# Kernel tuning notes

Measured on AMD Instinct MI355X. Metric: run time of the kernel, lower is better.

Reference implementation:

```python
import jax, jax.numpy as jnp
import numpy as np

THRESH = 1.0
TAU_M = 20.0
TAU_S = 5.0
NUM_STEPS = 300
CFG = (34 * 34 * 2, 800, 10)
BATCH = 32
SPIKE_PROB = 0.02


def _dtdu(um, us, spike):
    # dt/du = 1 / (du/dt) at spike time; du/dt = -um/tau_m + us/tau_s,
    # magnitude clamped away from zero for numerical safety.
    dudt = -um / TAU_M + us / TAU_S
    dudt = jnp.where(dudt >= 0, jnp.maximum(dudt, 1e-2), jnp.minimum(dudt, -1e-2))
    return spike / dudt


def _forward(input, W1, W2, batch_size):
    dm = jnp.exp(jnp.float32(-1.0 / TAU_M))
    ds = jnp.exp(jnp.float32(-1.0 / TAU_S))
    Din, H, O = CFG
    # (B,2,34,34,T) -> (T,B,Din)
    x = jnp.moveaxis(input.reshape(batch_size, Din, NUM_STEPS), -1, 0)
    z = lambda d: jnp.zeros((batch_size, d), jnp.float32)
    carry = (
        jnp.ones((batch_size, H), jnp.float32), z(Din), z(Din),   # sav1, vm1, vs1
        jnp.ones((batch_size, O), jnp.float32), z(H), z(H),       # sav2, vm2, vs2
        jnp.full((batch_size, O), float(NUM_STEPS), jnp.float32), # out_t
        z(O),                                                     # out_u
        jnp.zeros((3,), jnp.float32),                             # sum_sp
        jnp.zeros((batch_size, H, Din), jnp.float32),             # h1_v
        jnp.zeros((batch_size, O, H), jnp.float32),               # h2_v
        jnp.zeros((batch_size, H, Din), jnp.float32),             # h1_dvdt
        jnp.zeros((batch_size, O, H), jnp.float32),               # h2_dvdt
        z(H), z(O),                                               # h1_dtdu, h2_dtdu
    )

    def step(c, xs):
        (sav1, vm1, vs1, sav2, vm2, vs2, out_t, out_u, sum_sp,
         h1_v, h2_v, h1_dvdt, h2_dvdt, h1_dtdu, h2_dtdu) = c
        in_spike, t = xs
        # layer 1 NOSO neuron (dual-exponential kernel, single spike via sav gate)
        vm1 = vm1 * dm + in_spike
        vs1 = vs1 * ds + in_spike
        um1 = vm1 @ W1.T
        us1 = vs1 @ W1.T
        u1 = sav1 * (um1 - us1)
        spk1 = (u1 >= THRESH).astype(jnp.float32)
        sav1 = sav1 * (1.0 - spk1)
        # layer 2 (output neuron)
        vm2 = vm2 * dm + spk1
        vs2 = vs2 * ds + spk1
        um2 = vm2 @ W2.T
        us2 = vs2 @ W2.T
        u2 = sav2 * (um2 - us2)
        spk2 = (u2 >= THRESH).astype(jnp.float32)
        sav2 = sav2 * (1.0 - spk2)
        # spike-time / potential readout
        out_t = out_t + spk2 * (t.astype(jnp.float32) - NUM_STEPS)
        out_u = out_u + spk2 * u2
        sum_sp = sum_sp + jnp.stack([in_spike.sum(), spk1.sum(), spk2.sum()])
        # outer-product stat accumulation (B,out,in)
        h1_v = h1_v + spk1[:, :, None] * (vm1 - vs1)[:, None, :]
        h2_v = h2_v + spk2[:, :, None] * (vm2 - vs2)[:, None, :]
        h1_dvdt = h1_dvdt + spk1[:, :, None] * (vm1 / TAU_M - vs1 / TAU_S)[:, None, :]
        h2_dvdt = h2_dvdt + spk2[:, :, None] * (vm2 / TAU_M - vs2 / TAU_S)[:, None, :]
        h1_dtdu = h1_dtdu + _dtdu(um1, us1, spk1)
        h2_dtdu = h2_dtdu + _dtdu(um2, us2, spk2)
        return (sav1, vm1, vs1, sav2, vm2, vs2, out_t, out_u, sum_sp,
                h1_v, h2_v, h1_dvdt, h2_dvdt, h1_dtdu, h2_dtdu), None

    c, _ = jax.lax.scan(step, carry, (x, jnp.arange(NUM_STEPS)))
    out_t, out_u, sum_sp = c[6], c[7], c[8]
    h1_v, h2_v, h1_dvdt, h2_dvdt, h1_dtdu, h2_dtdu = c[9], c[10], c[11], c[12], c[13], c[14]
    return out_t, out_u, sum_sp, h1_v, h2_v, h1_dvdt, h2_dvdt, h1_dtdu, h2_dtdu


def setup_inputs() -> dict:
    key = jax.random.key(0)
    k1, k2, k3 = jax.random.split(key, 3)
    inp = (jax.random.uniform(k1, (BATCH, 2, 34, 34, NUM_STEPS)) < SPIKE_PROB).astype(jnp.float32)
    W1 = jax.random.normal(k2, (CFG[1], CFG[0]), jnp.float32) * float(np.sqrt(2.0 / CFG[0]))
    W2 = jax.random.normal(k3, (CFG[2], CFG[1]), jnp.float32) * float(np.sqrt(2.0 / CFG[1]))
    return {"input": inp, "W1": W1, "W2": W2, "batch_size": BATCH}


def reference(input, W1, W2, batch_size):
    return _forward(input, W1, W2, batch_size)
```

## Files before the change

kernel.cpp:

```cpp
#include <hip/hip_runtime.h>
#include <cstdint>
#include <cstddef>

#define BB 32
#define TT 300
#define DD 2312
#define HH 800
#define OO 10
#define CAP1 128
#define KMAX 32

typedef float f32x4 __attribute__((ext_vector_type(4)));

#define DM_F 0.95122942450071400909f
#define DS_F 0.81873075307798185867f

#define OUT_T_OFF 0
#define OUT_U_OFF 320
#define SUM_OFF   640
#define H1V_OFF   643ull
#define H2V_OFF   59187843ull
#define H1DV_OFF  59443843ull
#define H2DV_OFF  118631043ull
#define H1DT_OFF  118887043ull
#define H2DT_OFF  118912643ull

#define WS_W1T    0ull
#define WS_C1     7398400ull
#define WS_IDX1   38118400ull
#define WS_CNT1   55936000ull
#define WS_T1     56012800ull
#define WS_T2     56115200ull
#define WS_DMP    56116480ull
#define WS_DSP    56117760ull
#define WS_TIMES1 56119040ull

__global__ void k_pow(float* __restrict__ dmp, float* __restrict__ dsp) {
    if (threadIdx.x == 0) {
        float v = 1.f;
        for (int i = 0; i <= TT; ++i) { dmp[i] = v; v *= DM_F; }
    }
    if (threadIdx.x == 1) {
        float v = 1.f;
        for (int i = 0; i <= TT; ++i) { dsp[i] = v; v *= DS_F; }
    }
}

__global__ void k_transpose(const float* __restrict__ W1, float* __restrict__ W1T) {
    __shared__ float tile[32][33];
    int dx = blockIdx.x * 32, hy = blockIdx.y * 32;
    int tx = threadIdx.x, ty = threadIdx.y;
    int d = dx + tx, h = hy + ty;
    if (d < DD) tile[ty][tx] = W1[(size_t)h * DD + d];
    __syncthreads();
    int d2 = dx + ty, h2 = hy + tx;
    if (d2 < DD) W1T[(size_t)d2 * HH + h2] = tile[tx][ty];
}

__global__ void k_events(const float* __restrict__ in, int* __restrict__ cnt1,
                         unsigned short* __restrict__ idx1,
                         unsigned short* __restrict__ times1T) {
    int row = blockIdx.x * 4 + (threadIdx.x >> 6);
    int lane = threadIdx.x & 63;
    int b = row / DD, din = row - b * DD;
    const float* p = in + (size_t)row * TT;
    int kbase = 0;
    for (int r = 0; r < 5; ++r) {
        int t = r * 64 + lane;
        float v = (t < TT) ? p[t] : 0.f;
        bool act = (v != 0.f);
        unsigned long long m = __ballot(act);
        if (act) {
            int pos1 = atomicAdd(&cnt1[b * TT + t], 1);
            if (pos1 < CAP1) idx1[(size_t)(b * TT + t) * CAP1 + pos1] = (unsigned short)din;
            int pos = kbase + __popcll(m & ((1ull << lane) - 1ull));
            if (pos < KMAX)
                times1T[((size_t)b * KMAX + pos) * DD + din] = (unsigned short)t;
        }
        kbase += __popcll(m);
    }
    if (lane == 0 && kbase < KMAX)
        times1T[((size_t)b * KMAX + kbase) * DD + din] = 0xFFFFu;
}

__global__ __launch_bounds__(128) void k_c1(const int* __restrict__ cnt1,
                                            const unsigned short* __restrict__ idx1,
                                            const float* __restrict__ W1T,
                                            float* __restrict__ c1) {
    int blk = blockIdx.x % (BB * TT);
    int chunk = blockIdx.x / (BB * TT);
    int cnt = cnt1[blk];
    if (cnt > CAP1) cnt = CAP1;
    __shared__ int sidx[CAP1];
    for (int j = threadIdx.x; j < cnt; j += 128) sidx[j] = idx1[(size_t)blk * CAP1 + j];
    __syncthreads();
    int tid = threadIdx.x;
    if (tid < 100) {
        int v4i = chunk * 100 + tid;
        f32x4 acc = {0.f, 0.f, 0.f, 0.f};
        for (int j = 0; j < cnt; ++j) {
            const f32x4* row = (const f32x4*)(W1T + (size_t)sidx[j] * HH);
            acc += row[v4i];
        }
        ((f32x4*)(c1 + (size_t)blk * HH))[v4i] = acc;
    }
}

__global__ void k_scan1(const float* __restrict__ c1, int* __restrict__ t1,
                        float* __restrict__ out) {
    int id = blockIdx.x * 64 + threadIdx.x;
    int b = id / HH, h = id - b * HH;
    float um = 0.f, us = 0.f, umx = 0.f, usx = 0.f;
    int t1v = TT;
    const float* cbase = c1 + (size_t)b * TT * HH + h;
    #pragma unroll 4
    for (int t = 0; t < TT; ++t) {
        float c = cbase[(size_t)t * HH];
        um = um * DM_F + c;
        us = us * DS_F + c;
        bool cross = (um - us >= 1.0f) && (t1v == TT);
        t1v = cross ? t : t1v;
        umx = cross ? um : umx;
        usx = cross ? us : usx;
    }
    float dt = 0.f;
    if (t1v < TT) {
        float dudt = -umx / 20.0f + usx / 5.0f;
        dudt = (dudt >= 0.f) ? fmaxf(dudt, 1e-2f) : fminf(dudt, -1e-2f);
        dt = 1.f / dudt;
    }
    out[H1DT_OFF + (size_t)id] = dt;
    t1[id] = t1v;
}

__global__ __launch_bounds__(256) void k_layer2(const int* __restrict__ t1,
                                                const int* __restrict__ cnt1,
                                                const float* __restrict__ W2,
                                                int* __restrict__ t2,
                                                float* __restrict__ out) {
    __shared__ float c2[OO][TT];
    __shared__ int red[4];
    int b = blockIdx.x, tid = threadIdx.x;
    for (int i = tid; i < OO * TT; i += 256) ((float*)c2)[i] = 0.f;
    __syncthreads();
    for (int h = tid; h < HH; h += 256) {
        int t = t1[b * HH + h];
        if (t < TT) {
            #pragma unroll
            for (int o = 0; o < OO; ++o) atomicAdd(&c2[o][t], W2[o * HH + h]);
        }
    }
    __syncthreads();
    bool done = false;
    if (tid < OO) {
        float um = 0.f, us = 0.f, u2 = 0.f, dtdu = 0.f;
        int t2v = TT;
        for (int t = 0; t < TT; ++t) {
            float c = c2[tid][t];
            um = um * DM_F + c;
            us = us * DS_F + c;
            float u = um - us;
            if (u >= 1.0f) {
                done = true; t2v = t; u2 = u;
                float dudt = -um / 20.0f + us / 5.0f;
                dudt = (dudt >= 0.f) ? fmaxf(dudt, 1e-2f) : fminf(dudt, -1e-2f);
                dtdu = 1.f / dudt;
                break;
            }
        }
        out[OUT_T_OFF + b * OO + tid] = (float)t2v;
        out[OUT_U_OFF + b * OO + tid] = done ? u2 : 0.f;
        out[H2DT_OFF + (size_t)(b * OO + tid)] = done ? dtdu : 0.f;
        t2[b * OO + tid] = t2v;
    }
    unsigned long long m = __ballot(done);
    if (tid == 0 && m) atomicAdd(&out[SUM_OFF + 2], (float)__popcll(m));

    if (blockIdx.x == 0) {
        int s0 = 0, s1 = 0;
        for (int i = tid; i < BB * TT; i += 256) s0 += cnt1[i];
        for (int i = tid; i < BB * HH; i += 256) s1 += (t1[i] < TT);
        for (int d = 32; d >= 1; d >>= 1) {
            s0 += __shfl_down(s0, d, 64);
            s1 += __shfl_down(s1, d, 64);
        }
        int w = tid >> 6;
        if ((tid & 63) == 0) red[w] = s0;
        __syncthreads();
        if (tid == 0) out[SUM_OFF + 0] = (float)(red[0] + red[1] + red[2] + red[3]);
        __syncthreads();
        if ((tid & 63) == 0) red[w] = s1;
        __syncthreads();
        if (tid == 0) out[SUM_OFF + 1] = (float)(red[0] + red[1] + red[2] + red[3]);
    }
}

__global__ void k_h2(const int* __restrict__ t1, const int* __restrict__ t2,
                     const float* __restrict__ dmp, const float* __restrict__ dsp,
                     float* __restrict__ out) {
    int blk = blockIdx.x;
    int b = blk / OO;
    int t2v = t2[blk];
    bool spk = (t2v < TT);
    for (int h = threadIdx.x; h < HH; h += 256) {
        float v = 0.f, dv = 0.f;
        if (spk) {
            int t1v = t1[b * HH + h];
            if (t1v <= t2v) {
                int k = t2v - t1v;
                float a = dmp[k], s = dsp[k];
                v = a - s;
                dv = a / 20.0f - s / 5.0f;
            }
        }
        out[H2V_OFF + (size_t)blk * HH + h] = v;
        out[H2DV_OFF + (size_t)blk * HH + h] = dv;
    }
}

struct AS { float a, s; };

__device__ __forceinline__ AS h1_accum(const unsigned short* __restrict__ tp,
                                       int d, int t1v,
                                       const float* __restrict__ sm,
                                       const float* __restrict__ ss) {
    AS r; r.a = 0.f; r.s = 0.f;
    #pragma unroll 1
    for (int j = 0; j < KMAX; ++j) {
        int ts = tp[(size_t)j * DD + d];
        if (ts > t1v) break;
        int e = t1v - ts;
        r.a += sm[e]; r.s += ss[e];
    }
    return r;
}

__global__ __launch_bounds__(256) void k_h1ev(const int* __restrict__ t1,
                                              const unsigned short* __restrict__ times1T,
                                              const float* __restrict__ dmp,
                                              const float* __restrict__ dsp,
                                              float* __restrict__ out) {
    int blk = blockIdx.x;
    int b = blk / HH;
    int t1v = t1[blk];
    size_t rbase = (size_t)blk * DD;
    float* pv = out + H1V_OFF + rbase;
    float* pd = out + H1DV_OFF + rbase;
    int tid = threadIdx.x;
    if (t1v >= TT) {
        f32x4 z = {0.f, 0.f, 0.f, 0.f};
        for (int g = tid; g < 577; g += 256) {
            __builtin_nontemporal_store(z, (f32x4*)(pv + 1 + g * 4));
            __builtin_nontemporal_store(z, (f32x4*)(pd + 1 + g * 4));
        }
        if (tid < 4) {
            int d = (tid == 0) ? 0 : 2308 + tid;
            __builtin_nontemporal_store(0.f, pv + d);
            __builtin_nontemporal_store(0.f, pd + d);
        }
        return;
    }
    __shared__ float sm[TT], ss[TT];
    for (int i = tid; i < TT; i += 256) { sm[i] = dmp[i]; ss[i] = dsp[i]; }
    __syncthreads();
    const unsigned short* tp = times1T + (size_t)b * KMAX * DD;
    for (int g = tid; g < 577; g += 256) {
        int d0 = 1 + g * 4;
        AS r0 = h1_accum(tp, d0 + 0, t1v, sm, ss);
        AS r1 = h1_accum(tp, d0 + 1, t1v, sm, ss);
        AS r2 = h1_accum(tp, d0 + 2, t1v, sm, ss);
        AS r3 = h1_accum(tp, d0 + 3, t1v, sm, ss);
        f32x4 v4 = {r0.a - r0.s, r1.a - r1.s, r2.a - r2.s, r3.a - r3.s};
        f32x4 d4 = {r0.a * 0.05f - r0.s * 0.2f, r1.a * 0.05f - r1.s * 0.2f,
                    r2.a * 0.05f - r2.s * 0.2f, r3.a * 0.05f - r3.s * 0.2f};
        __builtin_nontemporal_store(v4, (f32x4*)(pv + d0));
        __builtin_nontemporal_store(d4, (f32x4*)(pd + d0));
    }
    if (tid < 4) {
        int d = (tid == 0) ? 0 : 2308 + tid;
        AS r = h1_accum(tp, d, t1v, sm, ss);
        __builtin_nontemporal_store(r.a - r.s, pv + d);
        __builtin_nontemporal_store(r.a * 0.05f - r.s * 0.2f, pd + d);
    }
}

extern "C" void kernel_launch(void* const* d_in, const int* in_sizes, int n_in,
                              void* d_out, int out_size, void* d_ws, size_t ws_size,
                              hipStream_t stream) {
    (void)in_sizes; (void)n_in; (void)out_size; (void)ws_size;
    const float* in = (const float*)d_in[0];
    const float* W1 = (const float*)d_in[1];
    const float* W2 = (const float*)d_in[2];
    float* out = (float*)d_out;
    char* ws = (char*)d_ws;

    float* W1T = (float*)(ws + WS_W1T);
    float* c1  = (float*)(ws + WS_C1);
    unsigned short* idx1 = (unsigned short*)(ws + WS_IDX1);
    int* cnt1 = (int*)(ws + WS_CNT1);
    int* t1   = (int*)(ws + WS_T1);
    int* t2   = (int*)(ws + WS_T2);
    float* dmp = (float*)(ws + WS_DMP);
    float* dsp = (float*)(ws + WS_DSP);
    unsigned short* times1T = (unsigned short*)(ws + WS_TIMES1);

    (void)hipMemsetAsync(cnt1, 0, (size_t)BB * TT * 4, stream);
    (void)hipMemsetAsync(out + SUM_OFF, 0, 3 * sizeof(float), stream);

    k_pow<<<1, 64, 0, stream>>>(dmp, dsp);
    k_transpose<<<dim3(73, 25), dim3(32, 32), 0, stream>>>(W1, W1T);
    k_events<<<(BB * DD) / 4, 256, 0, stream>>>(in, cnt1, idx1, times1T);
    k_c1<<<2 * BB * TT, 128, 0, stream>>>(cnt1, idx1, W1T, c1);
    k_scan1<<<(BB * HH) / 64, 64, 0, stream>>>(c1, t1, out);
    k_layer2<<<BB, 256, 0, stream>>>(t1, cnt1, W2, t2, out);
    k_h2<<<BB * OO, 256, 0, stream>>>(t1, t2, dmp, dsp, out);
    k_h1ev<<<BB * HH, 256, 0, stream>>>(t1, times1T, dmp, dsp, out);
}
```

Before: 434.4 us.

## Stage W1 row chunks in LDS for c1 gather, fuse small kernels

```diff
diff --git a/kernel.cpp b/kernel.cpp
--- a/kernel.cpp
+++ b/kernel.cpp
@@ -9,6 +9,8 @@
 #define OO 10
 #define CAP1 128
 #define KMAX 32
+#define HC 16
+#define NCHUNK (HH / HC)
 
 typedef float f32x4 __attribute__((ext_vector_type(4)));
 
@@ -25,41 +27,18 @@
 #define H1DT_OFF  118887043ull
 #define H2DT_OFF  118912643ull
 
-#define WS_W1T    0ull
 #define WS_C1     7398400ull
 #define WS_IDX1   38118400ull
 #define WS_CNT1   55936000ull
 #define WS_T1     56012800ull
-#define WS_T2     56115200ull
 #define WS_DMP    56116480ull
 #define WS_DSP    56117760ull
 #define WS_TIMES1 56119040ull
 
-__global__ void k_pow(float* __restrict__ dmp, float* __restrict__ dsp) {
-    if (threadIdx.x == 0) {
-        float v = 1.f;
-        for (int i = 0; i <= TT; ++i) { dmp[i] = v; v *= DM_F; }
-    }
-    if (threadIdx.x == 1) {
-        float v = 1.f;
-        for (int i = 0; i <= TT; ++i) { dsp[i] = v; v *= DS_F; }
-    }
-}
-
-__global__ void k_transpose(const float* __restrict__ W1, float* __restrict__ W1T) {
-    __shared__ float tile[32][33];
-    int dx = blockIdx.x * 32, hy = blockIdx.y * 32;
-    int tx = threadIdx.x, ty = threadIdx.y;
-    int d = dx + tx, h = hy + ty;
-    if (d < DD) tile[ty][tx] = W1[(size_t)h * DD + d];
-    __syncthreads();
-    int d2 = dx + ty, h2 = hy + tx;
-    if (d2 < DD) W1T[(size_t)d2 * HH + h2] = tile[tx][ty];
-}
-
 __global__ void k_events(const float* __restrict__ in, int* __restrict__ cnt1,
                          unsigned short* __restrict__ idx1,
-                         unsigned short* __restrict__ times1T) {
+                         unsigned short* __restrict__ times1T,
+                         float* __restrict__ dmp, float* __restrict__ dsp) {
     int row = blockIdx.x * 4 + (threadIdx.x >> 6);
     int lane = threadIdx.x & 63;
     int b = row / DD, din = row - b * DD;
@@ -81,28 +60,47 @@
     }
     if (lane == 0 && kbase < KMAX)
         times1T[((size_t)b * KMAX + kbase) * DD + din] = 0xFFFFu;
-}
-
-__global__ __launch_bounds__(128) void k_c1(const int* __restrict__ cnt1,
+    if (blockIdx.x == 0 && threadIdx.x < 2) {
+        float base = (threadIdx.x == 0) ? DM_F : DS_F;
+        float* tab = (threadIdx.x == 0) ? dmp : dsp;
+        float v = 1.f;
+        for (int i = 0; i <= TT; ++i) { tab[i] = v; v *= base; }
+    }
+}
+
+__global__ __launch_bounds__(320) void k_c1(const int* __restrict__ cnt1,
                                             const unsigned short* __restrict__ idx1,
-                                            const float* __restrict__ W1T,
+                                            const float* __restrict__ W1,
                                             float* __restrict__ c1) {
-    int blk = blockIdx.x % (BB * TT);
-    int chunk = blockIdx.x / (BB * TT);
+    __shared__ float tile[HC * DD];
+    int b = blockIdx.x & 31;
+    int chunk = blockIdx.x >> 5;
+    int h0 = chunk * HC;
+    int tid = threadIdx.x;
+    const f32x4* src = (const f32x4*)(W1 + (size_t)h0 * DD);
+    f32x4* dst = (f32x4*)tile;
+    for (int i = tid; i < HC * DD / 4; i += 320) dst[i] = src[i];
+    __syncthreads();
+    int t = tid;
+    if (t >= TT) return;
+    int blk = b * TT + t;
     int cnt = cnt1[blk];
     if (cnt > CAP1) cnt = CAP1;
-    __shared__ int sidx[CAP1];
-    for (int j = threadIdx.x; j < cnt; j += 128) sidx[j] = idx1[(size_t)blk * CAP1 + j];
-    __syncthreads();
-    int tid = threadIdx.x;
-    if (tid < 100) {
-        int v4i = chunk * 100 + tid;
-        f32x4 acc = {0.f, 0.f, 0.f, 0.f};
-        for (int j = 0; j < cnt; ++j) {
-            const f32x4* row = (const f32x4*)(W1T + (size_t)sidx[j] * HH);
-            acc += row[v4i];
-        }
-        ((f32x4*)(c1 + (size_t)blk * HH))[v4i] = acc;
+    const unsigned short* lp = idx1 + (size_t)blk * CAP1;
+    float acc[HC];
+    #pragma unroll
+    for (int c = 0; c < HC; ++c) acc[c] = 0.f;
+    #pragma unroll 4
+    for (int j = 0; j < cnt; ++j) {
+        int din = lp[j];
+        #pragma unroll
+        for (int c = 0; c < HC; ++c) acc[c] += tile[c * DD + din];
+    }
+    float* op = c1 + (size_t)blk * HH + h0;
+    #pragma unroll
+    for (int q = 0; q < HC / 4; ++q) {
+        f32x4 v = {acc[q * 4], acc[q * 4 + 1], acc[q * 4 + 2], acc[q * 4 + 3]};
+        ((f32x4*)op)[q] = v;
     }
 }
 
@@ -136,15 +134,19 @@
 __global__ __launch_bounds__(256) void k_layer2(const int* __restrict__ t1,
                                                 const int* __restrict__ cnt1,
                                                 const float* __restrict__ W2,
-                                                int* __restrict__ t2,
+                                                const float* __restrict__ dmp,
+                                                const float* __restrict__ dsp,
                                                 float* __restrict__ out) {
     __shared__ float c2[OO][TT];
+    __shared__ int t1s[HH];
+    __shared__ int t2s[OO];
     __shared__ int red[4];
     int b = blockIdx.x, tid = threadIdx.x;
     for (int i = tid; i < OO * TT; i += 256) ((float*)c2)[i] = 0.f;
+    for (int h = tid; h < HH; h += 256) t1s[h] = t1[b * HH + h];
     __syncthreads();
     for (int h = tid; h < HH; h += 256) {
-        int t = t1[b * HH + h];
+        int t = t1s[h];
         if (t < TT) {
             #pragma unroll
             for (int o = 0; o < OO; ++o) atomicAdd(&c2[o][t], W2[o * HH + h]);
@@ -171,10 +173,28 @@
         out[OUT_T_OFF + b * OO + tid] = (float)t2v;
         out[OUT_U_OFF + b * OO + tid] = done ? u2 : 0.f;
         out[H2DT_OFF + (size_t)(b * OO + tid)] = done ? dtdu : 0.f;
-        t2[b * OO + tid] = t2v;
+        t2s[tid] = t2v;
     }
     unsigned long long m = __ballot(done);
     if (tid == 0 && m) atomicAdd(&out[SUM_OFF + 2], (float)__popcll(m));
+    __syncthreads();
+    for (int i = tid; i < OO * HH; i += 256) {
+        int o = i / HH, h = i - o * HH;
+        int t2v = t2s[o];
+        float v = 0.f, dv = 0.f;
+        if (t2v < TT) {
+            int t1v = t1s[h];
+            if (t1v <= t2v) {
+                int k = t2v - t1v;
+                float a = dmp[k], s = dsp[k];
+                v = a - s;
+                dv = a * 0.05f - s * 0.2f;
+            }
+        }
+        size_t ro = (size_t)b * OO * HH + i;
+        out[H2V_OFF + ro] = v;
+        out[H2DV_OFF + ro] = dv;
+    }
 
     if (blockIdx.x == 0) {
         int s0 = 0, s1 = 0;
@@ -192,29 +212,6 @@
         if ((tid & 63) == 0) red[w] = s1;
         __syncthreads();
         if (tid == 0) out[SUM_OFF + 1] = (float)(red[0] + red[1] + red[2] + red[3]);
-    }
-}
-
-__global__ void k_h2(const int* __restrict__ t1, const int* __restrict__ t2,
-                     const float* __restrict__ dmp, const float* __restrict__ dsp,
-                     float* __restrict__ out) {
-    int blk = blockIdx.x;
-    int b = blk / OO;
-    int t2v = t2[blk];
-    bool spk = (t2v < TT);
-    for (int h = threadIdx.x; h < HH; h += 256) {
-        float v = 0.f, dv = 0.f;
-        if (spk) {
-            int t1v = t1[b * HH + h];
-            if (t1v <= t2v) {
-                int k = t2v - t1v;
-                float a = dmp[k], s = dsp[k];
-                v = a - s;
-                dv = a / 20.0f - s / 5.0f;
-            }
-        }
-        out[H2V_OFF + (size_t)blk * HH + h] = v;
-        out[H2DV_OFF + (size_t)blk * HH + h] = dv;
     }
 }
 
@@ -294,12 +291,10 @@
     float* out = (float*)d_out;
     char* ws = (char*)d_ws;
 
-    float* W1T = (float*)(ws + WS_W1T);
     float* c1  = (float*)(ws + WS_C1);
     unsigned short* idx1 = (unsigned short*)(ws + WS_IDX1);
     int* cnt1 = (int*)(ws + WS_CNT1);
     int* t1   = (int*)(ws + WS_T1);
-    int* t2   = (int*)(ws + WS_T2);
     float* dmp = (float*)(ws + WS_DMP);
     float* dsp = (float*)(ws + WS_DSP);
     unsigned short* times1T = (unsigned short*)(ws + WS_TIMES1);
@@ -307,12 +302,9 @@
     (void)hipMemsetAsync(cnt1, 0, (size_t)BB * TT * 4, stream);
     (void)hipMemsetAsync(out + SUM_OFF, 0, 3 * sizeof(float), stream);
 
-    k_pow<<<1, 64, 0, stream>>>(dmp, dsp);
-    k_transpose<<<dim3(73, 25), dim3(32, 32), 0, stream>>>(W1, W1T);
-    k_events<<<(BB * DD) / 4, 256, 0, stream>>>(in, cnt1, idx1, times1T);
-    k_c1<<<2 * BB * TT, 128, 0, stream>>>(cnt1, idx1, W1T, c1);
+    k_events<<<(BB * DD) / 4, 256, 0, stream>>>(in, cnt1, idx1, times1T, dmp, dsp);
+    k_c1<<<NCHUNK * BB, 320, 0, stream>>>(cnt1, idx1, W1, c1);
     k_scan1<<<(BB * HH) / 64, 64, 0, stream>>>(c1, t1, out);
-    k_layer2<<<BB, 256, 0, stream>>>(t1, cnt1, W2, t2, out);
-    k_h2<<<BB * OO, 256, 0, stream>>>(t1, t2, dmp, dsp, out);
+    k_layer2<<<BB, 256, 0, stream>>>(t1, cnt1, W2, dmp, dsp, out);
     k_h1ev<<<BB * HH, 256, 0, stream>>>(t1, times1T, dmp, dsp, out);
 }
```

Result: slower. 568.8 us (+30.9%).
